# Kernel tuning notes

Measured on AMD Instinct MI355X. Metric: run time of the kernel, lower is better.

Reference implementation:

```python
import jax, jax.numpy as jnp
import numpy as np

D_IN = 2048
D_OUT = 2048
CTX = 2048
N_HEADS = 16
HEAD_DIM = D_OUT // N_HEADS
ROPE_BASE = 10000.0


def precompute_rope(head_dim, context_length, base=ROPE_BASE):
    inv_freq = 1.0 / (base ** (jnp.arange(0, head_dim, 2, dtype=jnp.float32) / head_dim))
    pos = jnp.arange(context_length, dtype=jnp.float32)
    angles = pos[:, None] * inv_freq[None, :]            # (ctx, head_dim/2)
    angles = jnp.concatenate([angles, angles], axis=-1)  # (ctx, head_dim)
    return jnp.cos(angles), jnp.sin(angles)


def compute_rope(x, cos, sin):
    # x: (b, h, s, d)
    s = x.shape[2]
    d = x.shape[3]
    x1, x2 = x[..., : d // 2], x[..., d // 2 :]
    rotated = jnp.concatenate([-x2, x1], axis=-1)
    c = cos[:s][None, None, :, :]
    sn = sin[:s][None, None, :, :]
    return x * c + rotated * sn


def setup_inputs() -> dict:
    key = jax.random.key(0)
    kx, kq, kk, kv, ko = jax.random.split(key, 5)
    scale = 1.0 / np.sqrt(D_IN)
    return {
        "x": jax.random.normal(kx, (2, 2048, D_IN), dtype=jnp.float32),
        "W_query": jax.random.normal(kq, (D_IN, D_OUT), dtype=jnp.float32) * scale,
        "W_key": jax.random.normal(kk, (D_IN, D_OUT), dtype=jnp.float32) * scale,
        "W_value": jax.random.normal(kv, (D_IN, D_OUT), dtype=jnp.float32) * scale,
        "W_out": jax.random.normal(ko, (D_OUT, D_OUT), dtype=jnp.float32) * scale,
    }


def reference(x, W_query, W_key, W_value, W_out):
    b, s, _ = x.shape
    cos, sin = precompute_rope(HEAD_DIM, CTX)

    def split_heads(t):
        return t.reshape(b, s, N_HEADS, HEAD_DIM).transpose(0, 2, 1, 3)  # (b,h,s,d)

    q = split_heads(x @ W_query)
    k = split_heads(x @ W_key)
    v = split_heads(x @ W_value)

    q = compute_rope(q, cos, sin)
    k = compute_rope(k, cos, sin)

    scores = jnp.einsum("bhqd,bhkd->bhqk", q, k) / jnp.sqrt(jnp.float32(HEAD_DIM))
    causal = jnp.tril(jnp.ones((s, s), dtype=bool))
    scores = jnp.where(causal[None, None], scores, -jnp.inf)
    attn = jax.nn.softmax(scores, axis=-1)

    ctx = jnp.einsum("bhqk,bhkd->bhqd", attn, v)
    ctx = ctx.transpose(0, 2, 1, 3).reshape(b, s, D_OUT)
    return ctx @ W_out
```

## Files before the change

### kernel.cpp

```cpp
#include <hip/hip_runtime.h>
#include <hip/hip_bf16.h>

typedef __attribute__((ext_vector_type(8))) short bf16x8;
typedef __attribute__((ext_vector_type(4))) float f32x4;
typedef __attribute__((ext_vector_type(16))) float f32x16;
typedef __attribute__((ext_vector_type(4))) unsigned int u32x4;

__device__ inline unsigned short f2bf(float f) {
    unsigned int u = __builtin_bit_cast(unsigned int, f);
    u += 0x7FFFu + ((u >> 16) & 1u);
    return (unsigned short)(u >> 16);
}
__device__ inline float bf2f(unsigned short h) {
    unsigned int u = ((unsigned int)h) << 16;
    return __builtin_bit_cast(float, u);
}
__device__ inline unsigned int cvtpk(float lo, float hi) {
    unsigned int r;
    asm("v_cvt_pk_bf16_f32 %0, %1, %2" : "=v"(r) : "v"(lo), "v"(hi));
    return r;
}


__global__ void k_conv_x(const float* __restrict__ in, unsigned short* __restrict__ out, int n4) {
    int i = blockIdx.x * blockDim.x + threadIdx.x;
    if (i >= n4) return;
    float4 v = ((const float4*)in)[i];
    uint2 o;
    o.x = (unsigned)f2bf(v.x) | ((unsigned)f2bf(v.y) << 16);
    o.y = (unsigned)f2bf(v.z) | ((unsigned)f2bf(v.w) << 16);
    ((uint2*)out)[i] = o;
}

__global__ void k_wT(const float* __restrict__ w0, const float* __restrict__ w1,
                     const float* __restrict__ w2, const float* __restrict__ w3,
                     unsigned short* __restrict__ out) {
    __shared__ float tile[32][33];
    int z = blockIdx.z;
    const float* W = (z == 0) ? w0 : (z == 1) ? w1 : (z == 2) ? w2 : w3;
    unsigned short* O = out + (size_t)z * 2048 * 2048;
    int n0 = blockIdx.x * 32, k0 = blockIdx.y * 32;
    int tx = threadIdx.x & 31, ty = threadIdx.x >> 5;
#pragma unroll
    for (int j = 0; j < 4; ++j)
        tile[ty + j * 8][tx] = W[(size_t)(k0 + ty + j * 8) * 2048 + n0 + tx];
    __syncthreads();
#pragma unroll
    for (int j = 0; j < 4; ++j)
        O[(size_t)(n0 + ty + j * 8) * 2048 + k0 + tx] = f2bf(tile[tx][ty + j * 8]);
}

template <int OUT_MODE>
__global__ __launch_bounds__(256, 6) void gemm_bt(const unsigned short* __restrict__ A,
                                                  const unsigned short* __restrict__ Bt,
                                                  void* __restrict__ outp,
                                                  unsigned short* __restrict__ vtp,
                                                  int M, int N, int K) {
    __shared__ __align__(16) unsigned short As[128 * 64];
    __shared__ __align__(16) unsigned short Bs[128 * 64];
    const int tid = threadIdx.x, w = tid >> 6, l = tid & 63;
    const int m0 = blockIdx.y * 128, n0 = blockIdx.x * 128;
    const int wm = w >> 1, wn = w & 1;
    const int l15 = l & 15, lq = l >> 4;
    f32x4 acc[4][4] = {};
    const int lr = l >> 3, lg = l & 7;
    const int srcg = lg ^ lr;

    const int nkt = K >> 6;
    for (int kt = 0; kt < nkt; ++kt) {
        if (kt) __syncthreads();
#pragma unroll
        for (int i = 0; i < 4; ++i) {
            int r0 = (w * 4 + i) * 8;
            int row = r0 + lr;
            const unsigned short* sa = A + (size_t)(m0 + row) * K + kt * 64 + srcg * 8;
            __builtin_amdgcn_global_load_lds((const void*)sa, (void*)&As[(w * 4 + i) * 512], 16, 0, 0);
            const unsigned short* sb = Bt + (size_t)(n0 + row) * K + kt * 64 + srcg * 8;
            __builtin_amdgcn_global_load_lds((const void*)sb, (void*)&Bs[(w * 4 + i) * 512], 16, 0, 0);
        }
        __syncthreads();
#pragma unroll
        for (int kb = 0; kb < 2; ++kb) {
            bf16x8 af[4], bfr[4];
#pragma unroll
            for (int mi = 0; mi < 4; ++mi) {
                int row = wm * 64 + mi * 16 + l15;
                int g = (kb * 4 + lq) ^ (row & 7);
                af[mi] = *(const bf16x8*)&As[row * 64 + g * 8];
            }
#pragma unroll
            for (int ni = 0; ni < 4; ++ni) {
                int row = wn * 32 + (ni & 1) * 16 + (ni >> 1) * 64 + l15;
                int g = (kb * 4 + lq) ^ (row & 7);
                bfr[ni] = *(const bf16x8*)&Bs[row * 64 + g * 8];
            }
#pragma unroll
            for (int mi = 0; mi < 4; ++mi)
#pragma unroll
                for (int ni = 0; ni < 4; ++ni)
                    acc[mi][ni] = __builtin_amdgcn_mfma_f32_16x16x32_bf16(af[mi], bfr[ni],
                                                                          acc[mi][ni], 0, 0, 0);
        }
    }
    __builtin_amdgcn_sched_barrier(0);

    if constexpr (OUT_MODE == 0) {
        const int tsel = n0 >> 11, nloc = n0 & 2047;
        if (tsel < 2) {
            unsigned short* op = (unsigned short*)outp + (size_t)tsel * M * 2048;
            const float scale = (tsel == 0) ? 0.12751742f : 1.0f;
#pragma unroll
            for (int ni = 0; ni < 2; ++ni) {
                const int i = wn * 32 + ni * 16 + l15;
                const float rf =
                    __builtin_amdgcn_exp2f(-(float)i * 0.20762051f - 2.6514961f);
#pragma unroll
                for (int mi = 0; mi < 4; ++mi)
#pragma unroll
                    for (int r = 0; r < 4; ++r) {
                        int row = m0 + wm * 64 + mi * 16 + lq * 4 + r;
                        int sp = row & 2047;
                        float rev = __builtin_amdgcn_fractf((float)sp * rf);
                        float cs = __builtin_amdgcn_cosf(rev);
                        float sn = __builtin_amdgcn_sinf(rev);
                        float a = acc[mi][ni][r], bb = acc[mi][ni + 2][r];
                        op[(size_t)row * 2048 + nloc + i]      = f2bf((a * cs - bb * sn) * scale);
                        op[(size_t)row * 2048 + nloc + i + 64] = f2bf((bb * cs + a * sn) * scale);
                    }
            }
        } else {
            const int h = nloc >> 7;
            const int bsel = m0 >> 11;
            const int sp0 = (m0 & 2047) + wm * 64;
#pragma unroll
            for (int mi = 0; mi < 4; ++mi)
#pragma unroll
                for (int ni = 0; ni < 4; ++ni) {
                    int d = wn * 32 + (ni & 1) * 16 + (ni >> 1) * 64 + l15;
                    uint2 pv;
                    pv.x = cvtpk(acc[mi][ni][0], acc[mi][ni][1]);
                    pv.y = cvtpk(acc[mi][ni][2], acc[mi][ni][3]);
                    *(uint2*)&vtp[((size_t)((bsel * 16 + h) * 128 + d)) * 2048 + sp0 + mi * 16 + lq * 4] = pv;
                }
        }
    } else {
        float* op = (float*)outp;
#pragma unroll
        for (int mi = 0; mi < 4; ++mi)
#pragma unroll
            for (int ni = 0; ni < 4; ++ni)
#pragma unroll
                for (int r = 0; r < 4; ++r) {
                    int row = m0 + wm * 64 + mi * 16 + lq * 4 + r;
                    int col = n0 + wn * 32 + (ni & 1) * 16 + (ni >> 1) * 64 + l15;
                    op[(size_t)row * 2048 + col] = acc[mi][ni][r];
                }
    }
}

__global__ __launch_bounds__(256, 2) void k_attn(const unsigned short* __restrict__ Qp,
                                                 const unsigned short* __restrict__ Kp,
                                                 const unsigned short* __restrict__ VTp,
                                                 unsigned short* __restrict__ ctx) {
    __shared__ __align__(16) unsigned short Ks[2][64 * 128];
    __shared__ __align__(16) unsigned short Vs[2][128 * 64];
    const int tid = threadIdx.x, w = tid >> 6, l = tid & 63;
    const int l31 = l & 31, hi = l >> 5;
    const int x = blockIdx.x, bh = x & 31;
    const int xq = x >> 5;
    const int t = (xq < 8) ? (15 - xq) : (xq - 8);
    const int b = bh >> 4, h = bh & 15;
    const size_t b2048 = (size_t)b * 2048;
    const int h128 = h * 128;
    const size_t bh128 = (size_t)bh * 128;

    auto stage = [&](int kv) {
        const int bsel = kv & 1;
        const size_t kvoff = (size_t)kv * 64;
#pragma unroll
        for (int i = 0; i < 4; ++i) {
            int gi = w * 256 + i * 64 + l;
            int row = gi >> 4, g = gi & 15;
            int sg = g ^ (row & 7);
            const unsigned short* src = Kp + (b2048 + kvoff + row) * 2048 + h128 + sg * 8;
            __builtin_amdgcn_global_load_lds((const void*)src,
                                             (void*)&Ks[bsel][w * 2048 + i * 512], 16, 0, 0);
        }
#pragma unroll
        for (int i = 0; i < 4; ++i) {
            int gi = w * 256 + i * 64 + l;
            int row = gi >> 3, g = gi & 7;
            int sg = g ^ (row & 7);
            const unsigned short* src = VTp + (bh128 + row) * 2048 + kvoff + sg * 8;
            __builtin_amdgcn_global_load_lds((const void*)src,
                                             (void*)&Vs[bsel][w * 2048 + i * 512], 16, 0, 0);
        }
    };

    const int q0 = t * 128;
    const int wrow0 = q0 + w * 32;
    const int qg = wrow0 + l31;

    bf16x8 qf[8];
    {
        const unsigned short* qb = Qp + (b2048 + qg) * 2048 + h128 + hi * 8;
#pragma unroll
        for (int ds = 0; ds < 8; ++ds) qf[ds] = *(const bf16x8*)(qb + ds * 16);
#pragma unroll
        for (int ds = 0; ds < 8; ++ds) asm volatile("" ::"v"(qf[ds]));
    }
    f32x16 Oa[4] = {};
    float m2 = -1e30f, l2 = 0.f;
    const int kvmax = 2 * t + 1;

    stage(0);
    for (int kv = 0; kv <= kvmax; ++kv) {
        const int cur = kv & 1;
        if (kv < kvmax) {
            stage(kv + 1);
            asm volatile("s_waitcnt vmcnt(8)" ::: "memory");
        } else {
            asm volatile("s_waitcnt vmcnt(0)" ::: "memory");
        }
        __builtin_amdgcn_s_barrier();
        __builtin_amdgcn_sched_barrier(0);

        const int kvb = kv * 64;
        if (kvb <= wrow0 + 31) {
            f32x16 S[2] = {};
            __builtin_amdgcn_s_setprio(1);
#pragma unroll
            for (int ds = 0; ds < 8; ++ds)
#pragma unroll
                for (int st = 0; st < 2; ++st) {
                    int row = st * 32 + l31;
                    int g = (ds * 2 + hi) ^ (row & 7);
                    bf16x8 kf = *(const bf16x8*)&Ks[cur][row * 128 + g * 8];
                    S[st] = __builtin_amdgcn_mfma_f32_32x32x16_bf16(kf, qf[ds], S[st], 0, 0, 0);
                }
            __builtin_amdgcn_s_setprio(0);

            if (kvb + 63 > wrow0) {
#pragma unroll
                for (int st = 0; st < 2; ++st)
#pragma unroll
                    for (int r = 0; r < 16; ++r) {
                        int kpos = kvb + st * 32 + (r & 3) + 8 * (r >> 2) + 4 * hi;
                        if (kpos > qg) S[st][r] = -1e30f;
                    }
            }

            float pmax = -1e30f;
#pragma unroll
            for (int st = 0; st < 2; ++st)
#pragma unroll
                for (int r = 0; r < 16; ++r) pmax = fmaxf(pmax, S[st][r]);
            pmax = fmaxf(pmax, __shfl_xor(pmax, 32));
            if (__any(pmax > m2 + 8.0f)) {
                float mn = fmaxf(m2, pmax);
                float sc = __builtin_amdgcn_exp2f(m2 - mn);
                m2 = mn;
                l2 *= sc;
#pragma unroll
                for (int dt = 0; dt < 4; ++dt)
#pragma unroll
                    for (int e = 0; e < 16; ++e) Oa[dt][e] *= sc;
            }
            float rs = 0.f;
#pragma unroll
            for (int st = 0; st < 2; ++st)
#pragma unroll
                for (int r = 0; r < 16; ++r) {
                    float p = __builtin_amdgcn_exp2f(S[st][r] - m2);
                    S[st][r] = p;
                    rs += p;
                }
            rs += __shfl_xor(rs, 32);
            l2 += rs;

            bf16x8 pfrag[4];
#pragma unroll
            for (int ks = 0; ks < 4; ++ks) {
                const int st = ks >> 1, base = (ks & 1) * 8;
                unsigned int x0 = cvtpk(S[st][base + 0], S[st][base + 1]);
                unsigned int x1 = cvtpk(S[st][base + 2], S[st][base + 3]);
                unsigned int y0 = cvtpk(S[st][base + 4], S[st][base + 5]);
                unsigned int y1 = cvtpk(S[st][base + 6], S[st][base + 7]);
                unsigned int t0 = hi ? x0 : y0, t1 = hi ? x1 : y1;
                t0 = (unsigned int)__shfl_xor((int)t0, 32);
                t1 = (unsigned int)__shfl_xor((int)t1, 32);
                u32x4 fw;
                fw.x = hi ? t0 : x0;
                fw.y = hi ? t1 : x1;
                fw.z = hi ? y0 : t0;
                fw.w = hi ? y1 : t1;
                pfrag[ks] = __builtin_bit_cast(bf16x8, fw);
            }

            __builtin_amdgcn_s_setprio(1);
#pragma unroll
            for (int ks = 0; ks < 4; ++ks)
#pragma unroll
                for (int dt = 0; dt < 4; ++dt) {
                    int row = dt * 32 + l31;
                    int g = (ks * 2 + hi) ^ (row & 7);
                    bf16x8 vf = *(const bf16x8*)&Vs[cur][row * 64 + g * 8];
                    Oa[dt] = __builtin_amdgcn_mfma_f32_32x32x16_bf16(vf, pfrag[ks], Oa[dt], 0, 0, 0);
                }
            __builtin_amdgcn_s_setprio(0);
        }
        __builtin_amdgcn_sched_barrier(0);
        __builtin_amdgcn_s_barrier();
    }

    float inv = 1.0f / l2;
    unsigned short* cb = ctx + (b2048 + qg) * 2048 + h128;
#pragma unroll
    for (int dt = 0; dt < 4; ++dt)
#pragma unroll
        for (int g = 0; g < 4; ++g) {
            uint2 pv;
            pv.x = cvtpk(Oa[dt][4 * g + 0] * inv, Oa[dt][4 * g + 1] * inv);
            pv.y = cvtpk(Oa[dt][4 * g + 2] * inv, Oa[dt][4 * g + 3] * inv);
            *(uint2*)(cb + dt * 32 + 8 * g + 4 * hi) = pv;
        }
}


extern "C" void kernel_launch(void* const* d_in, const int* in_sizes, int n_in,
                              void* d_out, int out_size, void* d_ws, size_t ws_size,
                              hipStream_t stream) {
    const float* x  = (const float*)d_in[0];
    const float* wq = (const float*)d_in[1];
    const float* wk = (const float*)d_in[2];
    const float* wv = (const float*)d_in[3];
    const float* wo = (const float*)d_in[4];

    char* ws = (char*)d_ws;
    unsigned short* xb  = (unsigned short*)(ws);
    unsigned short* wT  = (unsigned short*)(ws + 16777216);
    unsigned short* qkv = (unsigned short*)(ws + 50331648);
    unsigned short* vT  = (unsigned short*)(ws + 100663296);
    unsigned short* ctx = xb;

    k_conv_x<<<8192, 256, 0, stream>>>(x, xb, 2097152);
    k_wT<<<dim3(64, 64, 4), 256, 0, stream>>>(wq, wk, wv, wo, wT);
    gemm_bt<0><<<dim3(48, 32), 256, 0, stream>>>(xb, wT, (void*)qkv, vT, 4096, 6144, 2048);
    k_attn<<<512, 256, 0, stream>>>(qkv, qkv + 8388608, vT, ctx);
    gemm_bt<1><<<dim3(16, 32), 256, 0, stream>>>(ctx, wT + (size_t)3 * 4194304, d_out, vT,
                                                 4096, 2048, 2048);
}
```

Baseline: 240.2 us.

## Software-pipeline attention: overlap next QK^T MFMA with current PV, triple-buffer V

Restructures the flash-attention loop so the QK^T scores for block kv+1 are computed in the same phase as the PV product for block kv. Softmax for the current block runs while the kv+2 loads are in flight. V gets a third LDS slot so its buffer lives across the extra stage, and loads are issued two blocks ahead. The aim is to hide softmax and exp latency behind MFMA work and keep the matrix units busy. In exchange it uses more LDS, which may limit occupancy at 2 blocks/CU, adds live registers for Sn, and makes the barrier/waitcnt logic more complex.

Result: no change. 240.1 us (-0.1%).

```diff
diff --git a/kernel.cpp b/kernel.cpp
--- a/kernel.cpp
+++ b/kernel.cpp
@@ -163,7 +163,7 @@
                                                  const unsigned short* __restrict__ VTp,
                                                  unsigned short* __restrict__ ctx) {
     __shared__ __align__(16) unsigned short Ks[2][64 * 128];
-    __shared__ __align__(16) unsigned short Vs[2][128 * 64];
+    __shared__ __align__(16) unsigned short Vs[3][128 * 64];
     const int tid = threadIdx.x, w = tid >> 6, l = tid & 63;
     const int l31 = l & 31, hi = l >> 5;
     const int x = blockIdx.x, bh = x & 31;
@@ -174,9 +174,9 @@
     const int h128 = h * 128;
     const size_t bh128 = (size_t)bh * 128;
 
-    auto stage = [&](int kv) {
-        const int bsel = kv & 1;
+    auto stageK = [&](int kv) {
         const size_t kvoff = (size_t)kv * 64;
+        unsigned short* kd = Ks[kv & 1];
 #pragma unroll
         for (int i = 0; i < 4; ++i) {
             int gi = w * 256 + i * 64 + l;
@@ -184,8 +184,12 @@
             int sg = g ^ (row & 7);
             const unsigned short* src = Kp + (b2048 + kvoff + row) * 2048 + h128 + sg * 8;
             __builtin_amdgcn_global_load_lds((const void*)src,
-                                             (void*)&Ks[bsel][w * 2048 + i * 512], 16, 0, 0);
-        }
+                                             (void*)&kd[w * 2048 + i * 512], 16, 0, 0);
+        }
+    };
+    auto stageV = [&](int kv, int slot) {
+        const size_t kvoff = (size_t)kv * 64;
+        unsigned short* vd = Vs[slot];
 #pragma unroll
         for (int i = 0; i < 4; ++i) {
             int gi = w * 256 + i * 64 + l;
@@ -193,12 +197,13 @@
             int sg = g ^ (row & 7);
             const unsigned short* src = VTp + (bh128 + row) * 2048 + kvoff + sg * 8;
             __builtin_amdgcn_global_load_lds((const void*)src,
-                                             (void*)&Vs[bsel][w * 2048 + i * 512], 16, 0, 0);
+                                             (void*)&vd[w * 2048 + i * 512], 16, 0, 0);
         }
     };
 
     const int q0 = t * 128;
     const int wrow0 = q0 + w * 32;
+    const int wlim = wrow0 + 31;
     const int qg = wrow0 + l31;
 
     bf16x8 qf[8];
@@ -213,43 +218,47 @@
     float m2 = -1e30f, l2 = 0.f;
     const int kvmax = 2 * t + 1;
 
-    stage(0);
+    stageK(0); stageV(0, 0);
+    stageK(1); stageV(1, 1);
+    asm volatile("s_waitcnt vmcnt(8)" ::: "memory");
+    __builtin_amdgcn_s_barrier();
+    __builtin_amdgcn_sched_barrier(0);
+
+    f32x16 S[2] = {};
+    {
+#pragma unroll
+        for (int ds = 0; ds < 8; ++ds)
+#pragma unroll
+            for (int st = 0; st < 2; ++st) {
+                int row = st * 32 + l31;
+                int g = (ds * 2 + hi) ^ (row & 7);
+                bf16x8 kf = *(const bf16x8*)&Ks[0][row * 128 + g * 8];
+                S[st] = __builtin_amdgcn_mfma_f32_32x32x16_bf16(kf, qf[ds], S[st], 0, 0, 0);
+            }
+        if (63 > wrow0) {
+#pragma unroll
+            for (int st = 0; st < 2; ++st)
+#pragma unroll
+                for (int r = 0; r < 16; ++r) {
+                    int kpos = st * 32 + (r & 3) + 8 * (r >> 2) + 4 * hi;
+                    if (kpos > qg) S[st][r] = -1e30f;
+                }
+        }
+    }
+    __builtin_amdgcn_s_barrier();
+
+    int vp = 0;
     for (int kv = 0; kv <= kvmax; ++kv) {
-        const int cur = kv & 1;
-        if (kv < kvmax) {
-            stage(kv + 1);
-            asm volatile("s_waitcnt vmcnt(8)" ::: "memory");
-        } else {
-            asm volatile("s_waitcnt vmcnt(0)" ::: "memory");
-        }
-        __builtin_amdgcn_s_barrier();
-        __builtin_amdgcn_sched_barrier(0);
-
-        const int kvb = kv * 64;
-        if (kvb <= wrow0 + 31) {
-            f32x16 S[2] = {};
-            __builtin_amdgcn_s_setprio(1);
-#pragma unroll
-            for (int ds = 0; ds < 8; ++ds)
-#pragma unroll
-                for (int st = 0; st < 2; ++st) {
-                    int row = st * 32 + l31;
-                    int g = (ds * 2 + hi) ^ (row & 7);
-                    bf16x8 kf = *(const bf16x8*)&Ks[cur][row * 128 + g * 8];
-                    S[st] = __builtin_amdgcn_mfma_f32_32x32x16_bf16(kf, qf[ds], S[st], 0, 0, 0);
-                }
-            __builtin_amdgcn_s_setprio(0);
-
-            if (kvb + 63 > wrow0) {
-#pragma unroll
-                for (int st = 0; st < 2; ++st)
-#pragma unroll
-                    for (int r = 0; r < 16; ++r) {
-                        int kpos = kvb + st * 32 + (r & 3) + 8 * (r >> 2) + 4 * hi;
-                        if (kpos > qg) S[st][r] = -1e30f;
-                    }
-            }
-
+        const bool act = (kv * 64 <= wlim);
+        const bool haveNext = (kv < kvmax);
+        if (kv + 2 <= kvmax) {
+            int s2 = vp + 2; if (s2 >= 3) s2 -= 3;
+            stageK(kv + 2);
+            stageV(kv + 2, s2);
+        }
+
+        bf16x8 pfrag[4];
+        if (act) {
             float pmax = -1e30f;
 #pragma unroll
             for (int st = 0; st < 2; ++st)
@@ -278,7 +287,6 @@
             rs += __shfl_xor(rs, 32);
             l2 += rs;
 
-            bf16x8 pfrag[4];
 #pragma unroll
             for (int ks = 0; ks < 4; ++ks) {
                 const int st = ks >> 1, base = (ks & 1) * 8;
@@ -296,21 +304,59 @@
                 fw.w = hi ? y1 : t1;
                 pfrag[ks] = __builtin_bit_cast(bf16x8, fw);
             }
-
-            __builtin_amdgcn_s_setprio(1);
+        }
+
+        if (kv + 2 <= kvmax) {
+            asm volatile("s_waitcnt vmcnt(8)" ::: "memory");
+        } else {
+            asm volatile("s_waitcnt vmcnt(0)" ::: "memory");
+        }
+        __builtin_amdgcn_s_barrier();
+        __builtin_amdgcn_sched_barrier(0);
+
+        f32x16 Sn[2] = {};
+        __builtin_amdgcn_s_setprio(1);
+        if (haveNext && (kv + 1) * 64 <= wlim) {
+            const unsigned short* kb = Ks[(kv + 1) & 1];
+#pragma unroll
+            for (int ds = 0; ds < 8; ++ds)
+#pragma unroll
+                for (int st = 0; st < 2; ++st) {
+                    int row = st * 32 + l31;
+                    int g = (ds * 2 + hi) ^ (row & 7);
+                    bf16x8 kf = *(const bf16x8*)&kb[row * 128 + g * 8];
+                    Sn[st] = __builtin_amdgcn_mfma_f32_32x32x16_bf16(kf, qf[ds], Sn[st], 0, 0, 0);
+                }
+        }
+        if (act) {
+            const unsigned short* vb = Vs[vp];
 #pragma unroll
             for (int ks = 0; ks < 4; ++ks)
 #pragma unroll
                 for (int dt = 0; dt < 4; ++dt) {
                     int row = dt * 32 + l31;
                     int g = (ks * 2 + hi) ^ (row & 7);
-                    bf16x8 vf = *(const bf16x8*)&Vs[cur][row * 64 + g * 8];
+                    bf16x8 vf = *(const bf16x8*)&vb[row * 64 + g * 8];
                     Oa[dt] = __builtin_amdgcn_mfma_f32_32x32x16_bf16(vf, pfrag[ks], Oa[dt], 0, 0, 0);
                 }
-            __builtin_amdgcn_s_setprio(0);
+        }
+        __builtin_amdgcn_s_setprio(0);
+
+        if (haveNext && (kv + 1) * 64 <= wlim && (kv + 1) * 64 + 63 > wrow0) {
+            const int kvb = (kv + 1) * 64;
+#pragma unroll
+            for (int st = 0; st < 2; ++st)
+#pragma unroll
+                for (int r = 0; r < 16; ++r) {
+                    int kpos = kvb + st * 32 + (r & 3) + 8 * (r >> 2) + 4 * hi;
+                    if (kpos > qg) Sn[st][r] = -1e30f;
+                }
         }
         __builtin_amdgcn_sched_barrier(0);
         __builtin_amdgcn_s_barrier();
+        S[0] = Sn[0];
+        S[1] = Sn[1];
+        ++vp; if (vp == 3) vp = 0;
     }
 
     float inv = 1.0f / l2;
```
